# Performance work log

Measured on AMD Instinct MI355X. Metric: run time of the kernel, lower is better.

## Reference

```python
import jax, jax.numpy as jnp
import numpy as np

HIDDEN = 2048
N_HEADS = 32
N_KV_HEADS = 8
HEAD_DIM = HIDDEN // N_HEADS  # 64
KV_DIM = N_KV_HEADS * HEAD_DIM  # 512


def setup_inputs() -> dict:
    key = jax.random.key(0)
    ks = jax.random.split(key, 9)
    s = 1.0 / np.sqrt(HIDDEN)
    x = jax.random.normal(ks[0], (2, 2048, HIDDEN), dtype=jnp.float32)
    wq = jax.random.uniform(ks[1], (HIDDEN, HIDDEN), jnp.float32, -s, s)
    bq = jax.random.uniform(ks[2], (HIDDEN,), jnp.float32, -s, s)
    wk = jax.random.uniform(ks[3], (KV_DIM, HIDDEN), jnp.float32, -s, s)
    bk = jax.random.uniform(ks[4], (KV_DIM,), jnp.float32, -s, s)
    wv = jax.random.uniform(ks[5], (KV_DIM, HIDDEN), jnp.float32, -s, s)
    bv = jax.random.uniform(ks[6], (KV_DIM,), jnp.float32, -s, s)
    wo = jax.random.uniform(ks[7], (HIDDEN, HIDDEN), jnp.float32, -s, s)
    bo = jax.random.uniform(ks[8], (HIDDEN,), jnp.float32, -s, s)
    return {"x": x, "wq": wq, "bq": bq, "wk": wk, "bk": bk,
            "wv": wv, "bv": bv, "wo": wo, "bo": bo}


def reference(x, wq, bq, wk, bk, wv, bv, wo, bo):
    B, S, _ = x.shape
    group = N_HEADS // N_KV_HEADS  # 4
    # projections (torch Linear: x @ W.T + b)
    q = (x @ wq.T + bq).reshape(B, S, N_HEADS, HEAD_DIM).transpose(0, 2, 1, 3)      # [B,H,S,D]
    k = (x @ wk.T + bk).reshape(B, S, N_KV_HEADS, HEAD_DIM).transpose(0, 2, 1, 3)   # [B,Hk,S,D]
    v = (x @ wv.T + bv).reshape(B, S, N_KV_HEADS, HEAD_DIM).transpose(0, 2, 1, 3)
    # repeat_interleave KV heads to match query heads
    k = jnp.repeat(k, group, axis=1)  # [B,H,S,D]
    v = jnp.repeat(v, group, axis=1)
    scale = 1.0 / np.sqrt(HEAD_DIM).astype(np.float32)
    attn = jnp.einsum('bhqd,bhkd->bhqk', q, k) * scale  # [B,H,S,S]
    score = jax.nn.softmax(attn, axis=-1)
    out = jnp.einsum('bhqk,bhkd->bhqd', score, v)       # [B,H,S,D]
    out = out.transpose(0, 2, 1, 3).reshape(B, S, HIDDEN)
    return out @ wo.T + bo
```

## Files before the change

### kernel.cpp

```cpp
#include <hip/hip_runtime.h>

typedef __attribute__((ext_vector_type(8))) short bf16x8;
typedef __attribute__((ext_vector_type(4))) float f32x4;
typedef __attribute__((ext_vector_type(16))) float f32x16;
typedef __attribute__((ext_vector_type(2))) float f32x2;

__device__ __forceinline__ short f2b(float f) {
  union { unsigned u; float f; } c;
  c.f = f;
  unsigned r = (c.u + 0x7FFFu + ((c.u >> 16) & 1u)) >> 16;
  return (short)r;
}

__device__ __forceinline__ int cvt_pk_bf16(float lo, float hi) {
  int r;
  asm("v_cvt_pk_bf16_f32 %0, %1, %2" : "=v"(r) : "v"(lo), "v"(hi));
  return r;
}

__device__ __forceinline__ void plswap(int& a, int& b) {
  asm("v_permlane32_swap_b32 %0, %1" : "+v"(a), "+v"(b));
}

__device__ __forceinline__ f32x2 pk_add(f32x2 a, f32x2 b) {
  f32x2 d;
  asm("v_pk_add_f32 %0, %1, %2" : "=v"(d) : "v"(a), "v"(b));
  return d;
}

__device__ __forceinline__ unsigned permb(unsigned s0, unsigned s1, unsigned sel) {
  unsigned d;
  asm("v_perm_b32 %0, %1, %2, %3" : "=v"(d) : "v"(s0), "v"(s1), "s"(sel));
  return d;
}

__device__ __forceinline__ void async16(const void* g, void* l) {
  __builtin_amdgcn_global_load_lds(
      (const __attribute__((address_space(1))) unsigned*)g,
      (__attribute__((address_space(3))) unsigned*)l, 16, 0, 0);
}

__global__ __launch_bounds__(256)
void conv_all(const float* __restrict__ x,  const float* __restrict__ wq,
              const float* __restrict__ wk, const float* __restrict__ wv,
              const float* __restrict__ wo, short* __restrict__ dst) {
  const size_t M = 1048576;
  size_t i = ((size_t)blockIdx.x * 256 + threadIdx.x) * 4;
  const float* src; size_t off;
  if (i < 8 * M)       { src = x;  off = 0; }
  else if (i < 12 * M) { src = wq; off = 8 * M; }
  else if (i < 13 * M) { src = wk; off = 12 * M; }
  else if (i < 14 * M) { src = wv; off = 13 * M; }
  else                 { src = wo; off = 14 * M; }
  float4 v = *(const float4*)(src + (i - off));
  short4 o;
  o.x = f2b(v.x); o.y = f2b(v.y); o.z = f2b(v.z); o.w = f2b(v.w);
  *(short4*)(dst + i) = o;
}

template <bool F32OUT>
__global__ __launch_bounds__(256)
void gemm_bt_bias(const short* __restrict__ A, const short* __restrict__ Bw,
                  const float* __restrict__ bias, void* __restrict__ Cv,
                  int M, int N, int K) {
  __shared__ short lsA[128 * 64];
  __shared__ short lsB[128 * 64];
  const int tid  = threadIdx.x;
  const int wave = tid >> 6, lane = tid & 63;
  const int l31  = lane & 31, hl = lane >> 5;
  const int GX  = gridDim.x;
  const int nwg = GX * gridDim.y;
  const int dd  = blockIdx.x + blockIdx.y * GX;
  const int logical = (dd & 7) * (nwg >> 3) + (dd >> 3);
  const int m0 = (logical / GX) * 128, n0 = (logical % GX) * 128;
  const int wm = (wave >> 1) * 64, wn = (wave & 1) * 64;

  f32x16 acc[2][2];
#pragma unroll
  for (int i = 0; i < 2; i++)
#pragma unroll
    for (int j = 0; j < 2; j++)
#pragma unroll
      for (int r = 0; r < 16; r++) acc[i][j][r] = 0.f;

  const int R  = tid >> 3;
  const int cs = tid & 7;
  const int gc = (cs ^ (R & 7)) << 3;
  const short* Arow[4]; const short* Brow[4];
#pragma unroll
  for (int b = 0; b < 4; b++) {
    Arow[b] = A  + (size_t)(m0 + R + 32 * b) * K + gc;
    Brow[b] = Bw + (size_t)(n0 + R + 32 * b) * K + gc;
  }
  const int ldst = R * 64 + cs * 8;

  for (int k0 = 0; k0 < K; k0 += 64) {
#pragma unroll
    for (int b = 0; b < 4; b++) {
      async16(Arow[b] + k0, lsA + ldst + b * 32 * 64);
      async16(Brow[b] + k0, lsB + ldst + b * 32 * 64);
    }
    __syncthreads();

    bf16x8 af[2][4], bfr[2][4];
#pragma unroll
    for (int i = 0; i < 2; i++) {
      const int Rr = wm + i * 32 + l31;
#pragma unroll
      for (int kq = 0; kq < 4; kq++) {
        const int c = kq * 2 + hl;
        af[i][kq] = *(const bf16x8*)(lsA + Rr * 64 + ((c ^ (Rr & 7)) << 3));
      }
    }
#pragma unroll
    for (int j = 0; j < 2; j++) {
      const int Sr = wn + j * 32 + l31;
#pragma unroll
      for (int kq = 0; kq < 4; kq++) {
        const int c = kq * 2 + hl;
        bfr[j][kq] = *(const bf16x8*)(lsB + Sr * 64 + ((c ^ (Sr & 7)) << 3));
      }
    }
#pragma unroll
    for (int kq = 0; kq < 4; kq++)
#pragma unroll
      for (int i = 0; i < 2; i++)
#pragma unroll
        for (int j = 0; j < 2; j++)
          acc[i][j] = __builtin_amdgcn_mfma_f32_32x32x16_bf16(
              af[i][kq], bfr[j][kq], acc[i][j], 0, 0, 0);
    __syncthreads();
  }

#pragma unroll
  for (int j = 0; j < 2; j++) {
    const int col = n0 + wn + j * 32 + l31;
    const float bb = bias[col];
#pragma unroll
    for (int i = 0; i < 2; i++) {
      const int rowb = m0 + wm + i * 32;
#pragma unroll
      for (int r = 0; r < 16; r++) {
        const int row = rowb + (r & 3) + 8 * (r >> 2) + 4 * hl;
        const float val = acc[i][j][r] + bb;
        if (F32OUT)
          ((float*)Cv)[(size_t)row * N + col] = val;
        else
          ((short*)Cv)[(size_t)row * N + col] = f2b(val);
      }
    }
  }
}

__global__ __launch_bounds__(256)
void gemm_qkv(const short* __restrict__ A, const short* __restrict__ Bw,
              const float* __restrict__ bq, const float* __restrict__ bk,
              const float* __restrict__ bv,
              short* __restrict__ Qo, short* __restrict__ Ko, short* __restrict__ Vo) {
  const int K = 2048;
  __shared__ short lsA[128 * 64];
  __shared__ short lsB[128 * 64];
  const int tid  = threadIdx.x;
  const int wave = tid >> 6, lane = tid & 63;
  const int l31  = lane & 31, hl = lane >> 5;
  const int GX  = gridDim.x;
  const int nwg = GX * gridDim.y;
  const int dd  = blockIdx.x + blockIdx.y * GX;
  const int logical = (dd & 7) * (nwg >> 3) + (dd >> 3);
  const int m0 = (logical / GX) * 128, n0 = (logical % GX) * 128;
  const int wm = (wave >> 1) * 64, wn = (wave & 1) * 64;

  f32x16 acc[2][2];
#pragma unroll
  for (int i = 0; i < 2; i++)
#pragma unroll
    for (int j = 0; j < 2; j++)
#pragma unroll
      for (int r = 0; r < 16; r++) acc[i][j][r] = 0.f;

  const int R  = tid >> 3;
  const int cs = tid & 7;
  const int gc = (cs ^ (R & 7)) << 3;
  const short* Arow[4]; const short* Brow[4];
#pragma unroll
  for (int b = 0; b < 4; b++) {
    Arow[b] = A  + (size_t)(m0 + R + 32 * b) * K + gc;
    Brow[b] = Bw + (size_t)(n0 + R + 32 * b) * K + gc;
  }
  const int ldst = R * 64 + cs * 8;

  for (int k0 = 0; k0 < K; k0 += 64) {
#pragma unroll
    for (int b = 0; b < 4; b++) {
      async16(Arow[b] + k0, lsA + ldst + b * 32 * 64);
      async16(Brow[b] + k0, lsB + ldst + b * 32 * 64);
    }
    __syncthreads();

    bf16x8 af[2][4], bfr[2][4];
#pragma unroll
    for (int i = 0; i < 2; i++) {
      const int Rr = wm + i * 32 + l31;
#pragma unroll
      for (int kq = 0; kq < 4; kq++) {
        const int c = kq * 2 + hl;
        af[i][kq] = *(const bf16x8*)(lsA + Rr * 64 + ((c ^ (Rr & 7)) << 3));
      }
    }
#pragma unroll
    for (int j = 0; j < 2; j++) {
      const int Sr = wn + j * 32 + l31;
#pragma unroll
      for (int kq = 0; kq < 4; kq++) {
        const int c = kq * 2 + hl;
        bfr[j][kq] = *(const bf16x8*)(lsB + Sr * 64 + ((c ^ (Sr & 7)) << 3));
      }
    }
#pragma unroll
    for (int kq = 0; kq < 4; kq++)
#pragma unroll
      for (int i = 0; i < 2; i++)
#pragma unroll
        for (int j = 0; j < 2; j++)
          acc[i][j] = __builtin_amdgcn_mfma_f32_32x32x16_bf16(
              af[i][kq], bfr[j][kq], acc[i][j], 0, 0, 0);
    __syncthreads();
  }

  short* base; int stride, coff; const float* bias;
  if (n0 < 2048)      { base = Qo; stride = 2048; bias = bq; coff = 0; }
  else if (n0 < 2560) { base = Ko; stride = 512;  bias = bk; coff = 2048; }
  else                { base = Vo; stride = 512;  bias = bv; coff = 2560; }
  const float qs = (n0 < 2048) ? 0.18033688011112043f : 1.0f;

#pragma unroll
  for (int j = 0; j < 2; j++) {
    const int lc = n0 + wn + j * 32 + l31 - coff;
    const float bb = bias[lc];
#pragma unroll
    for (int i = 0; i < 2; i++) {
      const int rowb = m0 + wm + i * 32;
#pragma unroll
      for (int r = 0; r < 16; r++) {
        const int row = rowb + (r & 3) + 8 * (r >> 2) + 4 * hl;
        base[(size_t)row * stride + lc] = f2b((acc[i][j][r] + bb) * qs);
      }
    }
  }
}

#define S_LEN 2048
#define HID   2048
#define KVD   512
#define ST    72

__global__ __launch_bounds__(256)
void gqa_flash(const short* __restrict__ Q, const short* __restrict__ Kb,
               const short* __restrict__ Vb, short* __restrict__ O) {
  __shared__ __align__(16) short lsK[64 * ST];
  __shared__ __align__(16) short lsVt[64 * ST];
  __shared__ float lsum[4][32];

  const int tid  = threadIdx.x;
  const int wave = tid >> 6, lane = tid & 63;
  const int l31  = lane & 31, hl = lane >> 5;

  const int d  = blockIdx.x + (blockIdx.y << 6);
  const int by = ((d & 7) << 1) | (d >> 9);
  const int qb = (d >> 3) & 63;
  const int b = by >> 3, kvh = by & 7;
  const int h = kvh * 4 + wave;
  const int q0 = qb * 32;

  const short* Qrow = Q + (size_t)(b * S_LEN + q0 + l31) * HID + h * 64 + hl * 8;
  bf16x8 qf[4];
#pragma unroll
  for (int f = 0; f < 4; f++) qf[f] = *(const bf16x8*)(Qrow + f * 16);

  f32x16 o0, o1;
#pragma unroll
  for (int i = 0; i < 16; i++) { o0[i] = 0.f; o1[i] = 0.f; }
  float lloc = 0.f;

  const short* Kp = Kb + (size_t)b * S_LEN * KVD + kvh * 64;
  const short* Vp = Vb + (size_t)b * S_LEN * KVD + kvh * 64;

  const int keyA = tid >> 3, chK = (tid & 7) * 8;
  const int kpV = tid & 31, dcV = (tid >> 5) * 8;

  bf16x8 kf0 = *(const bf16x8*)(Kp + (size_t)keyA * KVD + chK);
  bf16x8 kf1 = *(const bf16x8*)(Kp + (size_t)(keyA + 32) * KVD + chK);
  bf16x8 vf0 = *(const bf16x8*)(Vp + (size_t)(2 * kpV) * KVD + dcV);
  bf16x8 vf1 = *(const bf16x8*)(Vp + (size_t)(2 * kpV + 1) * KVD + dcV);

  for (int k0 = 0; k0 < S_LEN; k0 += 64) {
    *(bf16x8*)(lsK + keyA * ST + chK) = kf0;
    *(bf16x8*)(lsK + (keyA + 32) * ST + chK) = kf1;
    {
      const unsigned* u0 = (const unsigned*)&vf0;
      const unsigned* u1 = (const unsigned*)&vf1;
#pragma unroll
      for (int jw = 0; jw < 4; jw++) {
        unsigned lo = permb(u1[jw], u0[jw], 0x05040100u);
        unsigned hi = permb(u1[jw], u0[jw], 0x07060302u);
        *(unsigned*)(lsVt + (dcV + 2 * jw)     * ST + 2 * kpV) = lo;
        *(unsigned*)(lsVt + (dcV + 2 * jw + 1) * ST + 2 * kpV) = hi;
      }
    }
    __syncthreads();

    const int kn = (k0 + 64) & (S_LEN - 1);
    kf0 = *(const bf16x8*)(Kp + (size_t)(kn + keyA) * KVD + chK);
    kf1 = *(const bf16x8*)(Kp + (size_t)(kn + keyA + 32) * KVD + chK);
    vf0 = *(const bf16x8*)(Vp + (size_t)(kn + 2 * kpV) * KVD + dcV);
    vf1 = *(const bf16x8*)(Vp + (size_t)(kn + 2 * kpV + 1) * KVD + dcV);

    f32x16 s0, s1;
#pragma unroll
    for (int i = 0; i < 16; i++) { s0[i] = 0.f; s1[i] = 0.f; }
    __builtin_amdgcn_s_setprio(1);
#pragma unroll
    for (int f = 0; f < 4; f++) {
      bf16x8 ka = *(const bf16x8*)(lsK + l31 * ST + f * 16 + hl * 8);
      bf16x8 kb = *(const bf16x8*)(lsK + (32 + l31) * ST + f * 16 + hl * 8);
      s0 = __builtin_amdgcn_mfma_f32_32x32x16_bf16(ka, qf[f], s0, 0, 0, 0);
      s1 = __builtin_amdgcn_mfma_f32_32x32x16_bf16(kb, qf[f], s1, 0, 0, 0);
    }
    __builtin_amdgcn_s_setprio(0);

#pragma unroll
    for (int i = 0; i < 16; i++) {
      s0[i] = __builtin_amdgcn_exp2f(s0[i]);
      s1[i] = __builtin_amdgcn_exp2f(s1[i]);
    }
    {
      const f32x2* p0 = (const f32x2*)&s0;
      const f32x2* p1 = (const f32x2*)&s1;
      f32x2 t0 = pk_add(p0[0], p1[0]);
      f32x2 t1 = pk_add(p0[1], p1[1]);
      f32x2 t2 = pk_add(p0[2], p1[2]);
      f32x2 t3 = pk_add(p0[3], p1[3]);
      f32x2 t4 = pk_add(p0[4], p1[4]);
      f32x2 t5 = pk_add(p0[5], p1[5]);
      f32x2 t6 = pk_add(p0[6], p1[6]);
      f32x2 t7 = pk_add(p0[7], p1[7]);
      t0 = pk_add(t0, t4); t1 = pk_add(t1, t5);
      t2 = pk_add(t2, t6); t3 = pk_add(t3, t7);
      t0 = pk_add(t0, t2); t1 = pk_add(t1, t3);
      t0 = pk_add(t0, t1);
      lloc += t0.x + t0.y;
    }
    int P2[2][8];
#pragma unroll
    for (int qq = 0; qq < 8; qq++) {
      P2[0][qq] = cvt_pk_bf16(s0[2 * qq], s0[2 * qq + 1]);
      P2[1][qq] = cvt_pk_bf16(s1[2 * qq], s1[2 * qq + 1]);
    }

    __builtin_amdgcn_s_setprio(1);
#pragma unroll
    for (int t = 0; t < 4; t++) {
      const int j = t >> 1, b0 = (t & 1) * 4;
      int w0 = P2[j][b0 + 0], w2 = P2[j][b0 + 2];
      int w1 = P2[j][b0 + 1], w3 = P2[j][b0 + 3];
      plswap(w0, w2);
      plswap(w1, w3);
      union { unsigned u[4]; bf16x8 v; } pa;
      pa.u[0] = (unsigned)w0; pa.u[1] = (unsigned)w1;
      pa.u[2] = (unsigned)w2; pa.u[3] = (unsigned)w3;
      bf16x8 bv0 = *(const bf16x8*)(lsVt + l31 * ST + t * 16 + hl * 8);
      bf16x8 bv1 = *(const bf16x8*)(lsVt + (32 + l31) * ST + t * 16 + hl * 8);
      o0 = __builtin_amdgcn_mfma_f32_32x32x16_bf16(pa.v, bv0, o0, 0, 0, 0);
      o1 = __builtin_amdgcn_mfma_f32_32x32x16_bf16(pa.v, bv1, o1, 0, 0, 0);
    }
    __builtin_amdgcn_s_setprio(0);
    __syncthreads();
  }

  const float lfull = lloc + __shfl(lloc, lane ^ 32);
  if (lane < 32) lsum[wave][lane] = lfull;
#pragma unroll
  for (int r = 0; r < 16; r++) {
    const int qrow = (r & 3) + 8 * (r >> 2) + 4 * hl;
    const float rl = 1.0f / lsum[wave][qrow];
    short* op = O + (size_t)(b * S_LEN + q0 + qrow) * HID + h * 64 + l31;
    op[0]  = f2b(o0[r] * rl);
    op[32] = f2b(o1[r] * rl);
  }
}

extern "C" void kernel_launch(void* const* d_in, const int* in_sizes, int n_in,
                              void* d_out, int out_size, void* d_ws, size_t ws_size,
                              hipStream_t stream) {
  const float* x  = (const float*)d_in[0];
  const float* wq = (const float*)d_in[1];
  const float* bq = (const float*)d_in[2];
  const float* wk = (const float*)d_in[3];
  const float* bk = (const float*)d_in[4];
  const float* wv = (const float*)d_in[5];
  const float* bv = (const float*)d_in[6];
  const float* wo = (const float*)d_in[7];
  const float* bo = (const float*)d_in[8];
  float* out = (float*)d_out;

  short* xb  = (short*)d_ws;
  short* wqb = xb  + (size_t)4096 * 2048;
  short* wkb = wqb + (size_t)2048 * 2048;
  short* wvb = wkb + (size_t)512 * 2048;
  short* wob = wvb + (size_t)512 * 2048;
  short* Qb  = wob + (size_t)2048 * 2048;
  short* Kb  = Qb  + (size_t)4096 * 2048;
  short* Vb  = Kb  + (size_t)4096 * 512;
  short* AO  = Vb  + (size_t)4096 * 512;

  dim3 blk(256);
  conv_all<<<18 * 1048576 / 1024, blk, 0, stream>>>(x, wq, wk, wv, wo, xb);

  gemm_qkv<<<dim3(3072 / 128, 4096 / 128), blk, 0, stream>>>(xb, wqb, bq, bk, bv, Qb, Kb, Vb);
  gqa_flash<<<dim3(2048 / 32, 16), blk, 0, stream>>>(Qb, Kb, Vb, AO);
  gemm_bt_bias<true><<<dim3(2048 / 128, 4096 / 128), blk, 0, stream>>>(AO, wob, bo, out, 4096, 2048, 2048);
}
```

Before: 315.6 us.

## Double-buffer K/V shared tiles and split PV accumulators into even/odd chains

The flash attention loop now keeps two LDS buffers for K and transposed V. The next tile is written into the spare buffer while the current one is consumed, which drops one __syncthreads per iteration. The PV MFMA accumulation is also split into even and odd accumulator sets, summed at the end, to shorten the dependent MFMA chains. This doubles LDS use and adds 32 accumulator VGPRs, which may lower occupancy.

```diff
diff --git a/kernel.cpp b/kernel.cpp
--- a/kernel.cpp
+++ b/kernel.cpp
@@ -257,8 +257,8 @@
 __global__ __launch_bounds__(256)
 void gqa_flash(const short* __restrict__ Q, const short* __restrict__ Kb,
                const short* __restrict__ Vb, short* __restrict__ O) {
-  __shared__ __align__(16) short lsK[64 * ST];
-  __shared__ __align__(16) short lsVt[64 * ST];
+  __shared__ __align__(16) short lsK[2][64 * ST];
+  __shared__ __align__(16) short lsVt[2][64 * ST];
   __shared__ float lsum[4][32];
 
   const int tid  = threadIdx.x;
@@ -277,9 +277,9 @@
 #pragma unroll
   for (int f = 0; f < 4; f++) qf[f] = *(const bf16x8*)(Qrow + f * 16);
 
-  f32x16 o0, o1;
-#pragma unroll
-  for (int i = 0; i < 16; i++) { o0[i] = 0.f; o1[i] = 0.f; }
+  f32x16 o0e, o0o, o1e, o1o;
+#pragma unroll
+  for (int i = 0; i < 16; i++) { o0e[i] = 0.f; o0o[i] = 0.f; o1e[i] = 0.f; o1o[i] = 0.f; }
   float lloc = 0.f;
 
   const short* Kp = Kb + (size_t)b * S_LEN * KVD + kvh * 64;
@@ -288,32 +288,37 @@
   const int keyA = tid >> 3, chK = (tid & 7) * 8;
   const int kpV = tid & 31, dcV = (tid >> 5) * 8;
 
-  bf16x8 kf0 = *(const bf16x8*)(Kp + (size_t)keyA * KVD + chK);
-  bf16x8 kf1 = *(const bf16x8*)(Kp + (size_t)(keyA + 32) * KVD + chK);
-  bf16x8 vf0 = *(const bf16x8*)(Vp + (size_t)(2 * kpV) * KVD + dcV);
-  bf16x8 vf1 = *(const bf16x8*)(Vp + (size_t)(2 * kpV + 1) * KVD + dcV);
-
-  for (int k0 = 0; k0 < S_LEN; k0 += 64) {
-    *(bf16x8*)(lsK + keyA * ST + chK) = kf0;
-    *(bf16x8*)(lsK + (keyA + 32) * ST + chK) = kf1;
-    {
-      const unsigned* u0 = (const unsigned*)&vf0;
-      const unsigned* u1 = (const unsigned*)&vf1;
-#pragma unroll
-      for (int jw = 0; jw < 4; jw++) {
-        unsigned lo = permb(u1[jw], u0[jw], 0x05040100u);
-        unsigned hi = permb(u1[jw], u0[jw], 0x07060302u);
-        *(unsigned*)(lsVt + (dcV + 2 * jw)     * ST + 2 * kpV) = lo;
-        *(unsigned*)(lsVt + (dcV + 2 * jw + 1) * ST + 2 * kpV) = hi;
-      }
-    }
-    __syncthreads();
-
-    const int kn = (k0 + 64) & (S_LEN - 1);
+  bf16x8 kf0, kf1, vf0, vf1;
+  auto prefetch = [&](int kt) {
+    const int kn = (kt * 64) & (S_LEN - 1);
     kf0 = *(const bf16x8*)(Kp + (size_t)(kn + keyA) * KVD + chK);
     kf1 = *(const bf16x8*)(Kp + (size_t)(kn + keyA + 32) * KVD + chK);
     vf0 = *(const bf16x8*)(Vp + (size_t)(kn + 2 * kpV) * KVD + dcV);
     vf1 = *(const bf16x8*)(Vp + (size_t)(kn + 2 * kpV + 1) * KVD + dcV);
+  };
+  auto commit = [&](int bs) {
+    *(bf16x8*)(lsK[bs] + keyA * ST + chK) = kf0;
+    *(bf16x8*)(lsK[bs] + (keyA + 32) * ST + chK) = kf1;
+    const unsigned* u0 = (const unsigned*)&vf0;
+    const unsigned* u1 = (const unsigned*)&vf1;
+#pragma unroll
+    for (int jw = 0; jw < 4; jw++) {
+      unsigned lo = permb(u1[jw], u0[jw], 0x05040100u);
+      unsigned hi = permb(u1[jw], u0[jw], 0x07060302u);
+      *(unsigned*)(lsVt[bs] + (dcV + 2 * jw)     * ST + 2 * kpV) = lo;
+      *(unsigned*)(lsVt[bs] + (dcV + 2 * jw + 1) * ST + 2 * kpV) = hi;
+    }
+  };
+
+  prefetch(0);
+  commit(0);
+  prefetch(1);
+  __syncthreads();
+
+  for (int t = 0; t < S_LEN / 64; t++) {
+    const int bs = t & 1;
+    commit(bs ^ 1);
+    prefetch(t + 2);
 
     f32x16 s0, s1;
 #pragma unroll
@@ -321,8 +326,8 @@
     __builtin_amdgcn_s_setprio(1);
 #pragma unroll
     for (int f = 0; f < 4; f++) {
-      bf16x8 ka = *(const bf16x8*)(lsK + l31 * ST + f * 16 + hl * 8);
-      bf16x8 kb = *(const bf16x8*)(lsK + (32 + l31) * ST + f * 16 + hl * 8);
+      bf16x8 ka = *(const bf16x8*)(lsK[bs] + l31 * ST + f * 16 + hl * 8);
+      bf16x8 kb = *(const bf16x8*)(lsK[bs] + (32 + l31) * ST + f * 16 + hl * 8);
       s0 = __builtin_amdgcn_mfma_f32_32x32x16_bf16(ka, qf[f], s0, 0, 0, 0);
       s1 = __builtin_amdgcn_mfma_f32_32x32x16_bf16(kb, qf[f], s1, 0, 0, 0);
     }
@@ -359,8 +364,8 @@
 
     __builtin_amdgcn_s_setprio(1);
 #pragma unroll
-    for (int t = 0; t < 4; t++) {
-      const int j = t >> 1, b0 = (t & 1) * 4;
+    for (int tt = 0; tt < 4; tt++) {
+      const int j = tt >> 1, b0 = (tt & 1) * 4;
       int w0 = P2[j][b0 + 0], w2 = P2[j][b0 + 2];
       int w1 = P2[j][b0 + 1], w3 = P2[j][b0 + 3];
       plswap(w0, w2);
@@ -368,15 +373,22 @@
       union { unsigned u[4]; bf16x8 v; } pa;
       pa.u[0] = (unsigned)w0; pa.u[1] = (unsigned)w1;
       pa.u[2] = (unsigned)w2; pa.u[3] = (unsigned)w3;
-      bf16x8 bv0 = *(const bf16x8*)(lsVt + l31 * ST + t * 16 + hl * 8);
-      bf16x8 bv1 = *(const bf16x8*)(lsVt + (32 + l31) * ST + t * 16 + hl * 8);
-      o0 = __builtin_amdgcn_mfma_f32_32x32x16_bf16(pa.v, bv0, o0, 0, 0, 0);
-      o1 = __builtin_amdgcn_mfma_f32_32x32x16_bf16(pa.v, bv1, o1, 0, 0, 0);
+      bf16x8 bv0 = *(const bf16x8*)(lsVt[bs] + l31 * ST + tt * 16 + hl * 8);
+      bf16x8 bv1 = *(const bf16x8*)(lsVt[bs] + (32 + l31) * ST + tt * 16 + hl * 8);
+      if (tt & 1) {
+        o0o = __builtin_amdgcn_mfma_f32_32x32x16_bf16(pa.v, bv0, o0o, 0, 0, 0);
+        o1o = __builtin_amdgcn_mfma_f32_32x32x16_bf16(pa.v, bv1, o1o, 0, 0, 0);
+      } else {
+        o0e = __builtin_amdgcn_mfma_f32_32x32x16_bf16(pa.v, bv0, o0e, 0, 0, 0);
+        o1e = __builtin_amdgcn_mfma_f32_32x32x16_bf16(pa.v, bv1, o1e, 0, 0, 0);
+      }
     }
     __builtin_amdgcn_s_setprio(0);
     __syncthreads();
   }
 
+  f32x16 o0 = o0e + o0o;
+  f32x16 o1 = o1e + o1o;
   const float lfull = lloc + __shfl(lloc, lane ^ 32);
   if (lane < 32) lsum[wave][lane] = lfull;
 #pragma unroll
```

Measured after the change: 319.5 us. Within noise of the previous version (+1.2%).

## Load K fragments directly from global into registers, bypassing LDS

Applied to the files above, without the earlier changes.

Each wave now loads its own K MFMA operand fragments straight from global memory into registers, prefetching the next tile after the QK MFMAs, instead of staging K through shared memory. V staging is restructured into prefetch and commit steps, with an extra barrier per iteration. This removes the LDS writes and reads for K and halves LDS use. In exchange, each of the 4 waves reloads the same K tile from global/L2, uses more registers for the K prefetch, and adds a second sync per iteration.

```diff
diff --git a/kernel.cpp b/kernel.cpp
--- a/kernel.cpp
+++ b/kernel.cpp
@@ -257,7 +257,6 @@
 __global__ __launch_bounds__(256)
 void gqa_flash(const short* __restrict__ Q, const short* __restrict__ Kb,
                const short* __restrict__ Vb, short* __restrict__ O) {
-  __shared__ __align__(16) short lsK[64 * ST];
   __shared__ __align__(16) short lsVt[64 * ST];
   __shared__ float lsum[4][32];
 
@@ -285,48 +284,56 @@
   const short* Kp = Kb + (size_t)b * S_LEN * KVD + kvh * 64;
   const short* Vp = Vb + (size_t)b * S_LEN * KVD + kvh * 64;
 
-  const int keyA = tid >> 3, chK = (tid & 7) * 8;
+  const short* Kfp = Kp + (size_t)l31 * KVD + hl * 8;
   const int kpV = tid & 31, dcV = (tid >> 5) * 8;
 
-  bf16x8 kf0 = *(const bf16x8*)(Kp + (size_t)keyA * KVD + chK);
-  bf16x8 kf1 = *(const bf16x8*)(Kp + (size_t)(keyA + 32) * KVD + chK);
-  bf16x8 vf0 = *(const bf16x8*)(Vp + (size_t)(2 * kpV) * KVD + dcV);
-  bf16x8 vf1 = *(const bf16x8*)(Vp + (size_t)(2 * kpV + 1) * KVD + dcV);
-
-  for (int k0 = 0; k0 < S_LEN; k0 += 64) {
-    *(bf16x8*)(lsK + keyA * ST + chK) = kf0;
-    *(bf16x8*)(lsK + (keyA + 32) * ST + chK) = kf1;
-    {
-      const unsigned* u0 = (const unsigned*)&vf0;
-      const unsigned* u1 = (const unsigned*)&vf1;
-#pragma unroll
-      for (int jw = 0; jw < 4; jw++) {
-        unsigned lo = permb(u1[jw], u0[jw], 0x05040100u);
-        unsigned hi = permb(u1[jw], u0[jw], 0x07060302u);
-        *(unsigned*)(lsVt + (dcV + 2 * jw)     * ST + 2 * kpV) = lo;
-        *(unsigned*)(lsVt + (dcV + 2 * jw + 1) * ST + 2 * kpV) = hi;
-      }
-    }
-    __syncthreads();
-
-    const int kn = (k0 + 64) & (S_LEN - 1);
-    kf0 = *(const bf16x8*)(Kp + (size_t)(kn + keyA) * KVD + chK);
-    kf1 = *(const bf16x8*)(Kp + (size_t)(kn + keyA + 32) * KVD + chK);
+  bf16x8 kr[2][4];
+  auto kload = [&](int kt) {
+    const int kn = (kt * 64) & (S_LEN - 1);
+    const short* base = Kfp + (size_t)kn * KVD;
+#pragma unroll
+    for (int half = 0; half < 2; half++)
+#pragma unroll
+      for (int f = 0; f < 4; f++)
+        kr[half][f] = *(const bf16x8*)(base + half * 32 * KVD + f * 16);
+  };
+
+  bf16x8 vf0, vf1;
+  auto vprefetch = [&](int kt) {
+    const int kn = (kt * 64) & (S_LEN - 1);
     vf0 = *(const bf16x8*)(Vp + (size_t)(kn + 2 * kpV) * KVD + dcV);
     vf1 = *(const bf16x8*)(Vp + (size_t)(kn + 2 * kpV + 1) * KVD + dcV);
-
+  };
+  auto vcommit = [&]() {
+    const unsigned* u0 = (const unsigned*)&vf0;
+    const unsigned* u1 = (const unsigned*)&vf1;
+#pragma unroll
+    for (int jw = 0; jw < 4; jw++) {
+      unsigned lo = permb(u1[jw], u0[jw], 0x05040100u);
+      unsigned hi = permb(u1[jw], u0[jw], 0x07060302u);
+      *(unsigned*)(lsVt + (dcV + 2 * jw)     * ST + 2 * kpV) = lo;
+      *(unsigned*)(lsVt + (dcV + 2 * jw + 1) * ST + 2 * kpV) = hi;
+    }
+  };
+
+  kload(0);
+  vprefetch(0);
+  vcommit();
+  __syncthreads();
+  vprefetch(1);
+
+  for (int t = 0; t < S_LEN / 64; t++) {
     f32x16 s0, s1;
 #pragma unroll
     for (int i = 0; i < 16; i++) { s0[i] = 0.f; s1[i] = 0.f; }
     __builtin_amdgcn_s_setprio(1);
 #pragma unroll
     for (int f = 0; f < 4; f++) {
-      bf16x8 ka = *(const bf16x8*)(lsK + l31 * ST + f * 16 + hl * 8);
-      bf16x8 kb = *(const bf16x8*)(lsK + (32 + l31) * ST + f * 16 + hl * 8);
-      s0 = __builtin_amdgcn_mfma_f32_32x32x16_bf16(ka, qf[f], s0, 0, 0, 0);
-      s1 = __builtin_amdgcn_mfma_f32_32x32x16_bf16(kb, qf[f], s1, 0, 0, 0);
+      s0 = __builtin_amdgcn_mfma_f32_32x32x16_bf16(kr[0][f], qf[f], s0, 0, 0, 0);
+      s1 = __builtin_amdgcn_mfma_f32_32x32x16_bf16(kr[1][f], qf[f], s1, 0, 0, 0);
     }
     __builtin_amdgcn_s_setprio(0);
+    kload(t + 1);
 
 #pragma unroll
     for (int i = 0; i < 16; i++) {
@@ -359,8 +366,8 @@
 
     __builtin_amdgcn_s_setprio(1);
 #pragma unroll
-    for (int t = 0; t < 4; t++) {
-      const int j = t >> 1, b0 = (t & 1) * 4;
+    for (int tt = 0; tt < 4; tt++) {
+      const int j = tt >> 1, b0 = (tt & 1) * 4;
       int w0 = P2[j][b0 + 0], w2 = P2[j][b0 + 2];
       int w1 = P2[j][b0 + 1], w3 = P2[j][b0 + 3];
       plswap(w0, w2);
@@ -368,13 +375,18 @@
       union { unsigned u[4]; bf16x8 v; } pa;
       pa.u[0] = (unsigned)w0; pa.u[1] = (unsigned)w1;
       pa.u[2] = (unsigned)w2; pa.u[3] = (unsigned)w3;
-      bf16x8 bv0 = *(const bf16x8*)(lsVt + l31 * ST + t * 16 + hl * 8);
-      bf16x8 bv1 = *(const bf16x8*)(lsVt + (32 + l31) * ST + t * 16 + hl * 8);
+      bf16x8 bv0 = *(const bf16x8*)(lsVt + l31 * ST + tt * 16 + hl * 8);
+      bf16x8 bv1 = *(const bf16x8*)(lsVt + (32 + l31) * ST + tt * 16 + hl * 8);
       o0 = __builtin_amdgcn_mfma_f32_32x32x16_bf16(pa.v, bv0, o0, 0, 0, 0);
       o1 = __builtin_amdgcn_mfma_f32_32x32x16_bf16(pa.v, bv1, o1, 0, 0, 0);
     }
     __builtin_amdgcn_s_setprio(0);
     __syncthreads();
+    if (t < S_LEN / 64 - 1) {
+      vcommit();
+      __syncthreads();
+      vprefetch(t + 2);
+    }
   }
 
   const float lfull = lloc + __shfl(lloc, lane ^ 32);
```

Result: slower. 372.0 us (+17.8%).
